# Kernel optimization log

Measured on AMD Instinct MI355X. Metric: run time of the kernel, lower is better.

The kernel has to match this reference:

```python
import jax, jax.numpy as jnp
import numpy as np

N_NODES = 50000
N_EDGES = 800000


def sage_conv(x, src, dst, Wl, b, Wr, n_nodes):
    # mean aggregation of source-node features into target nodes
    msg = x[src]                                            # [E, d]
    agg = jax.ops.segment_sum(msg, dst, num_segments=n_nodes)  # [N, d]
    cnt = jax.ops.segment_sum(jnp.ones((src.shape[0],), x.dtype), dst,
                              num_segments=n_nodes)         # [N]
    agg = agg / jnp.maximum(cnt, 1.0)[:, None]
    # out = lin_l(mean_aggr) + lin_r(x); bias only on lin_l (PyG default)
    return agg @ Wl.T + b + x @ Wr.T


def setup_inputs() -> dict:
    key = jax.random.key(0)
    ks = jax.random.split(key, 10)
    d_in, d_h, d_out = 128, 128, 64
    sc = lambda k, shp: jax.random.normal(k, shp, jnp.float32) * (1.0 / np.sqrt(shp[-1]))
    return {
        "x": jax.random.normal(ks[0], (N_NODES, d_in), jnp.float32),
        "edge_index": jax.random.randint(ks[1], (2, N_EDGES), 0, N_NODES, jnp.int64),
        "W1l": sc(ks[2], (d_h, d_in)), "b1": jnp.zeros((d_h,), jnp.float32),
        "W1r": sc(ks[3], (d_h, d_in)),
        "W2l": sc(ks[4], (d_h, d_h)), "b2": jnp.zeros((d_h,), jnp.float32),
        "W2r": sc(ks[5], (d_h, d_h)),
        "W3l": sc(ks[6], (d_out, d_h)), "b3": jnp.zeros((d_out,), jnp.float32),
        "W3r": sc(ks[7], (d_out, d_h)),
    }


def reference(x, edge_index, W1l, b1, W1r, W2l, b2, W2r, W3l, b3, W3r):
    src, dst = edge_index[0], edge_index[1]
    n = x.shape[0]
    # layer 1 + relu (dropout is identity in eval mode)
    h = jax.nn.relu(sage_conv(x, src, dst, W1l, b1, W1r, n))
    # layer 2 + relu
    h = jax.nn.relu(sage_conv(h, src, dst, W2l, b2, W2r, n))
    # final layer, no activation
    return sage_conv(h, src, dst, W3l, b3, W3r, n)
```

## Files before the change

### kernel.cpp

```cpp
#include <hip/hip_runtime.h>
#include <hip/hip_bf16.h>

#define DIN 128

typedef __attribute__((ext_vector_type(8))) short short8;
typedef __attribute__((ext_vector_type(4))) float f32x4;
typedef __attribute__((ext_vector_type(4))) unsigned short ushort4v;
typedef __attribute__((ext_vector_type(8))) unsigned short ushort8v;

__device__ __forceinline__ unsigned short f2bf(float f) {
    unsigned int u = __float_as_uint(f);
    u += 0x7FFFu + ((u >> 16) & 1u);
    return (unsigned short)(u >> 16);
}
__device__ __forceinline__ float bflo(unsigned int v) { return __uint_as_float(v << 16); }
__device__ __forceinline__ float bfhi(unsigned int v) { return __uint_as_float(v & 0xFFFF0000u); }

#define PAD 32
#define CHUNK 4096

__device__ __forceinline__ void pack_w_body(const float* __restrict__ Wl,
                                            const float* __restrict__ Wr,
                                            unsigned short* __restrict__ Wp, int NT, int idx) {
    if (idx >= NT * 8 * 64) return;
    int l = idx & 63;
    int ts = idx >> 6;
    int ks = ts & 7;
    int nt = ts >> 3;
    int row = nt * 16 + (l & 15);
    int k = ks * 32 + ((l >> 4) << 3);
    const float* s = (k < 128) ? (Wl + (size_t)row * 128 + k)
                               : (Wr + (size_t)row * 128 + (k - 128));
    float4 v0 = *reinterpret_cast<const float4*>(s);
    float4 v1 = *reinterpret_cast<const float4*>(s + 4);
    unsigned short* d = Wp + (size_t)idx * 8;
    ushort4v o0 = {f2bf(v0.x), f2bf(v0.y), f2bf(v0.z), f2bf(v0.w)};
    ushort4v o1 = {f2bf(v1.x), f2bf(v1.y), f2bf(v1.z), f2bf(v1.w)};
    *reinterpret_cast<ushort4v*>(d) = o0;
    *reinterpret_cast<ushort4v*>(d + 4) = o1;
}

__global__ __launch_bounds__(256) void prep_kernel(
    const float* __restrict__ x, unsigned short* __restrict__ xb,
    const float* __restrict__ W1l, const float* __restrict__ W1r, unsigned short* __restrict__ Wp1,
    const float* __restrict__ W2l, const float* __restrict__ W2r, unsigned short* __restrict__ Wp2,
    const float* __restrict__ W3l, const float* __restrict__ W3r, unsigned short* __restrict__ Wp3,
    const int* __restrict__ dst, int* __restrict__ bcnt, int E, int n, int CB) {
    __shared__ int h[256];
    int t = threadIdx.x;
    int b = blockIdx.x;
    if (b < CB) {
        int i = b * 256 + t;
        if (i < n * 16) {
            int node = i >> 4;
            int f0 = (i & 15) << 3;
            const float* s = x + (size_t)node * DIN + f0;
            float4 v0 = *reinterpret_cast<const float4*>(s);
            float4 v1 = *reinterpret_cast<const float4*>(s + 4);
            ushort8v o = {f2bf(v0.x), f2bf(v0.y), f2bf(v0.z), f2bf(v0.w),
                          f2bf(v1.x), f2bf(v1.y), f2bf(v1.z), f2bf(v1.w)};
            *reinterpret_cast<ushort8v*>(xb + (size_t)(f0 >> 5) * n * 32 +
                                         (size_t)node * 32 + (f0 & 31)) = o;
        }
        return;
    }
    b -= CB;
    if (b < 16) { pack_w_body(W1l, W1r, Wp1, 8, b * 256 + t); return; }
    b -= 16;
    if (b < 16) { pack_w_body(W2l, W2r, Wp2, 8, b * 256 + t); return; }
    b -= 16;
    if (b < 8) { pack_w_body(W3l, W3r, Wp3, 4, b * 256 + t); return; }
    b -= 8;
    h[t] = 0;
    __syncthreads();
    for (int i = b * 256 + t; i < E; i += 784 * 256)
        atomicAdd(&h[dst[i] >> 8], 1);
    __syncthreads();
    if (h[t] > 0) atomicAdd(&bcnt[t * PAD], h[t]);
}

__global__ __launch_bounds__(256) void bucket_scan_kernel(const int* __restrict__ bcnt,
                                                          int* __restrict__ bbase,
                                                          int* __restrict__ bcur,
                                                          int* __restrict__ row_ptr,
                                                          int nb, int n, int E) {
    __shared__ int s[256];
    int t = threadIdx.x;
    int v = (t < nb) ? bcnt[t * PAD] : 0;
    s[t] = v;
    __syncthreads();
    for (int off = 1; off < 256; off <<= 1) {
        int add = (t >= off) ? s[t - off] : 0;
        __syncthreads();
        s[t] += add;
        __syncthreads();
    }
    int excl = s[t] - v;
    bbase[t] = excl;
    bcur[t * PAD] = excl;
    if (t == 255) {
        bbase[256] = s[255];
        row_ptr[n] = E;
    }
}

__global__ __launch_bounds__(256) void chunk_scatter_kernel(const int* __restrict__ src,
                                                            const int* __restrict__ dst,
                                                            int* __restrict__ bcur,
                                                            unsigned int* __restrict__ tmp,
                                                            int E) {
    __shared__ int hist[256];
    __shared__ int base[256];
    int t = threadIdx.x;
    int e0 = blockIdx.x * CHUNK;
    int e1 = min(e0 + CHUNK, E);
    hist[t] = 0;
    __syncthreads();
    for (int e = e0 + t; e < e1; e += 256) {
        atomicAdd(&hist[dst[e] >> 8], 1);
    }
    __syncthreads();
    int hh = hist[t];
    if (hh > 0) base[t] = atomicAdd(&bcur[t * PAD], hh);
    __syncthreads();
    hist[t] = 0;
    __syncthreads();
    for (int e = e0 + t; e < e1; e += 256) {
        int d = dst[e];
        int bb = d >> 8;
        int p = base[bb] + atomicAdd(&hist[bb], 1);
        tmp[p] = (unsigned int)src[e] | ((unsigned int)(d & 255) << 16);
    }
}

__global__ __launch_bounds__(256) void bucket_fill_kernel(const unsigned int* __restrict__ tmp,
                                                          const int* __restrict__ bbase,
                                                          int* __restrict__ row_ptr,
                                                          unsigned short* __restrict__ col,
                                                          int n) {
    int b = blockIdx.x;
    int node0 = b << 8;
    int nn = min(256, n - node0);
    int begB = bbase[b], endB = bbase[b + 1];
    __shared__ int s[256];
    __shared__ int cur[256];
    int t = threadIdx.x;
    s[t] = 0;
    __syncthreads();
    for (int i = begB + t; i < endB; i += 256)
        atomicAdd(&s[(tmp[i] >> 16) & 255], 1);
    __syncthreads();
    int v = s[t];
    __syncthreads();
    for (int off = 1; off < 256; off <<= 1) {
        int add = (t >= off) ? s[t - off] : 0;
        __syncthreads();
        s[t] += add;
        __syncthreads();
    }
    int r = begB + s[t] - v;
    if (t < nn) row_ptr[node0 + t] = r;
    cur[t] = r;
    __syncthreads();
    for (int i = begB + t; i < endB; i += 256) {
        unsigned int e = tmp[i];
        int p = atomicAdd(&cur[(e >> 16) & 255], 1);
        col[p] = (unsigned short)(e & 0xFFFFu);
    }
}

__global__ __launch_bounds__(256) void aggregate_kernel(const unsigned short* __restrict__ feat,
                                                        const int* __restrict__ row_ptr,
                                                        const unsigned short* __restrict__ col,
                                                        unsigned short* __restrict__ agg,
                                                        int n, int nbn2) {
    int b = blockIdx.x;
    int chunk = (b >> 1) & 3;
    int nb = (b >> 3) * 2 + (b & 1);
    int lane = threadIdx.x & 63;
    int wave = threadIdx.x >> 6;
    int q = lane >> 4;
    int node = nb * 16 + wave * 4 + q;
    int slot = (lane >> 2) & 3;
    int fb = (lane & 3) << 3;
    size_t cs = (size_t)n * 32;
    const unsigned short* fc = feat + (size_t)chunk * cs;

    int beg = 0, end = 0;
    if (node < n) { beg = row_ptr[node]; end = row_ptr[node + 1]; }
    float a0 = 0.f, a1 = 0.f, a2 = 0.f, a3 = 0.f, a4 = 0.f, a5 = 0.f, a6 = 0.f, a7 = 0.f;
    int e = beg + slot;
    for (; e + 4 < end; e += 8) {
        int c0 = col[e];
        int c1 = col[e + 4];
        uint4 v0 = *reinterpret_cast<const uint4*>(fc + (size_t)c0 * 32 + fb);
        uint4 v1 = *reinterpret_cast<const uint4*>(fc + (size_t)c1 * 32 + fb);
        a0 += bflo(v0.x); a1 += bfhi(v0.x); a2 += bflo(v0.y); a3 += bfhi(v0.y);
        a4 += bflo(v0.z); a5 += bfhi(v0.z); a6 += bflo(v0.w); a7 += bfhi(v0.w);
        a0 += bflo(v1.x); a1 += bfhi(v1.x); a2 += bflo(v1.y); a3 += bfhi(v1.y);
        a4 += bflo(v1.z); a5 += bfhi(v1.z); a6 += bflo(v1.w); a7 += bfhi(v1.w);
    }
    if (e < end) {
        int c0 = col[e];
        uint4 v0 = *reinterpret_cast<const uint4*>(fc + (size_t)c0 * 32 + fb);
        a0 += bflo(v0.x); a1 += bfhi(v0.x); a2 += bflo(v0.y); a3 += bfhi(v0.y);
        a4 += bflo(v0.z); a5 += bfhi(v0.z); a6 += bflo(v0.w); a7 += bfhi(v0.w);
    }
    a0 += __shfl_xor(a0, 4); a1 += __shfl_xor(a1, 4); a2 += __shfl_xor(a2, 4);
    a3 += __shfl_xor(a3, 4); a4 += __shfl_xor(a4, 4); a5 += __shfl_xor(a5, 4);
    a6 += __shfl_xor(a6, 4); a7 += __shfl_xor(a7, 4);
    a0 += __shfl_xor(a0, 8); a1 += __shfl_xor(a1, 8); a2 += __shfl_xor(a2, 8);
    a3 += __shfl_xor(a3, 8); a4 += __shfl_xor(a4, 8); a5 += __shfl_xor(a5, 8);
    a6 += __shfl_xor(a6, 8); a7 += __shfl_xor(a7, 8);
    if (slot == 0 && node < n) {
        float sc = 1.0f / fmaxf((float)(end - beg), 1.0f);
        ushort8v o = {f2bf(a0 * sc), f2bf(a1 * sc), f2bf(a2 * sc), f2bf(a3 * sc),
                      f2bf(a4 * sc), f2bf(a5 * sc), f2bf(a6 * sc), f2bf(a7 * sc)};
        *reinterpret_cast<ushort8v*>(agg + (size_t)chunk * cs + (size_t)node * 32 + fb) = o;
    }
}

template <int DOUT, bool RELU, bool OUTBF>
__global__ __launch_bounds__(256, 4) void mfma_gemm_kernel(
    const unsigned short* __restrict__ aggb, const unsigned short* __restrict__ xb,
    const unsigned short* __restrict__ Wp, const float* __restrict__ bias,
    void* __restrict__ outv, int n) {
    constexpr int NT = DOUT / 16;
    const int lane = threadIdx.x & 63;
    const int wave = threadIdx.x >> 6;
    const int row0 = blockIdx.x * 64 + wave * 16;
    const int ar = row0 + (lane & 15);
    const int kg = (lane >> 4) << 3;
    const bool ok = ar < n;
    const size_t cs = (size_t)n * 32;

    const short8 z = {0, 0, 0, 0, 0, 0, 0, 0};
    short8 a[8];
    const unsigned short* arow = aggb + (size_t)ar * 32 + kg;
    const unsigned short* xrow = xb + (size_t)ar * 32 + kg;
#pragma unroll
    for (int ks = 0; ks < 4; ks++)
        a[ks] = ok ? *reinterpret_cast<const short8*>(arow + ks * cs) : z;
#pragma unroll
    for (int ks = 0; ks < 4; ks++)
        a[4 + ks] = ok ? *reinterpret_cast<const short8*>(xrow + ks * cs) : z;

    f32x4 acc[NT];
#pragma unroll
    for (int nt = 0; nt < NT; nt++) acc[nt] = {0.f, 0.f, 0.f, 0.f};

    const unsigned short* wp = Wp + ((size_t)lane << 3);
#pragma unroll
    for (int nt = 0; nt < NT; nt++) {
#pragma unroll
        for (int ks = 0; ks < 8; ks++) {
            short8 b = *reinterpret_cast<const short8*>(wp + ((size_t)(nt * 8 + ks) << 9));
            acc[nt] = __builtin_amdgcn_mfma_f32_16x16x32_bf16(a[ks], b, acc[nt], 0, 0, 0);
        }
    }

    const int orow0 = row0 + ((lane >> 4) << 2);
#pragma unroll
    for (int nt = 0; nt < NT; nt++) {
        int c = nt * 16 + (lane & 15);
        float bv = bias[c];
#pragma unroll
        for (int rg = 0; rg < 4; rg++) {
            int rr = orow0 + rg;
            if (rr < n) {
                float v = acc[nt][rg] + bv;
                if (RELU) v = fmaxf(v, 0.f);
                if (OUTBF) {
                    reinterpret_cast<unsigned short*>(outv)[(size_t)(nt >> 1) * cs +
                                                            (size_t)rr * 32 +
                                                            ((nt & 1) * 16 + (lane & 15))] =
                        f2bf(v);
                } else {
                    reinterpret_cast<float*>(outv)[(size_t)rr * DOUT + c] = v;
                }
            }
        }
    }
}

extern "C" void kernel_launch(void* const* d_in, const int* in_sizes, int n_in,
                              void* d_out, int out_size, void* d_ws, size_t ws_size,
                              hipStream_t stream) {
    const float* x = (const float*)d_in[0];
    const int* ei = (const int*)d_in[1];
    const float* W1l = (const float*)d_in[2];
    const float* b1 = (const float*)d_in[3];
    const float* W1r = (const float*)d_in[4];
    const float* W2l = (const float*)d_in[5];
    const float* b2 = (const float*)d_in[6];
    const float* W2r = (const float*)d_in[7];
    const float* W3l = (const float*)d_in[8];
    const float* b3 = (const float*)d_in[9];
    const float* W3r = (const float*)d_in[10];
    float* out = (float*)d_out;

    const int n = in_sizes[0] / DIN;
    const int E = in_sizes[1] / 2;
    const int* src = ei;
    const int* dst = ei + E;

    char* p = (char*)d_ws;
    auto take = [&](size_t bytes) {
        char* r = p;
        p += (bytes + 255) & ~(size_t)255;
        return r;
    };
    int* bcnt = (int*)take(256 * PAD * 4);
    int* bcur = (int*)take(256 * PAD * 4);
    int* bbase = (int*)take(257 * 4);
    int* row_ptr = (int*)take(((size_t)n + 1) * 4);
    unsigned int* tmp = (unsigned int*)take((size_t)E * 4);
    unsigned short* col = (unsigned short*)take((size_t)E * 2);
    unsigned short* xb = (unsigned short*)take((size_t)n * DIN * 2);
    unsigned short* aggb = (unsigned short*)take((size_t)n * DIN * 2);
    unsigned short* h1b = (unsigned short*)take((size_t)n * DIN * 2);
    unsigned short* h2b = (unsigned short*)take((size_t)n * DIN * 2);
    unsigned short* Wp1 = (unsigned short*)take(128 * 256 * 2);
    unsigned short* Wp2 = (unsigned short*)take(128 * 256 * 2);
    unsigned short* Wp3 = (unsigned short*)take(64 * 256 * 2);

    const int n_buckets = (n + 255) / 256;
    const int nbn = (n + 15) / 16;
    const int nbn2 = (nbn + 1) & ~1;
    const int nb_agg = 4 * nbn2;
    const int nb_gemm = (n + 63) / 64;
    const int nb_chunk = (E + CHUNK - 1) / CHUNK;
    const int CB = (n * 16 + 255) / 256;
    const int nb_prep = CB + 16 + 16 + 8 + 784;

    hipMemsetAsync(bcnt, 0, 256 * PAD * 4, stream);
    prep_kernel<<<nb_prep, 256, 0, stream>>>(x, xb, W1l, W1r, Wp1, W2l, W2r, Wp2,
                                             W3l, W3r, Wp3, dst, bcnt, E, n, CB);

    bucket_scan_kernel<<<1, 256, 0, stream>>>(bcnt, bbase, bcur, row_ptr, n_buckets, n, E);
    chunk_scatter_kernel<<<nb_chunk, 256, 0, stream>>>(src, dst, bcur, tmp, E);
    bucket_fill_kernel<<<n_buckets, 256, 0, stream>>>(tmp, bbase, row_ptr, col, n);

    aggregate_kernel<<<nb_agg, 256, 0, stream>>>(xb, row_ptr, col, aggb, n, nbn2);
    mfma_gemm_kernel<128, true, true><<<nb_gemm, 256, 0, stream>>>(aggb, xb, Wp1, b1, h1b, n);

    aggregate_kernel<<<nb_agg, 256, 0, stream>>>(h1b, row_ptr, col, aggb, n, nbn2);
    mfma_gemm_kernel<128, true, true><<<nb_gemm, 256, 0, stream>>>(aggb, h1b, Wp2, b2, h2b, n);

    aggregate_kernel<<<nb_agg, 256, 0, stream>>>(h2b, row_ptr, col, aggb, n, nbn2);
    mfma_gemm_kernel<64, false, false><<<nb_gemm, 256, 0, stream>>>(aggb, h2b, Wp3, b3, out, n);
}
```

Baseline: 187.4 us.

## Transform before aggregating in final layer and fold bucket scan into CSR kernels

The final SAGE layer now applies both weight matrices first: W3l·h goes to a 64-wide bf16 buffer and W3r·h + bias to a float buffer. A new agg_add kernel then mean-aggregates the 64-wide projected features and adds the residual, halving the width of the last gather. The separate single-block bucket scan kernel is removed; each scatter and fill block recomputes the small 256-entry prefix scan, and bcur becomes a zero-initialised relative offset. The aggregation loop is also unrolled to four gathers per iteration for more memory-level parallelism. In exchange the last layer rounds the projected messages to bf16 before averaging, and every block does redundant scan work.

```diff
diff --git a/kernel.cpp b/kernel.cpp
--- a/kernel.cpp
+++ b/kernel.cpp
@@ -79,39 +79,26 @@
     if (h[t] > 0) atomicAdd(&bcnt[t * PAD], h[t]);
 }
 
-__global__ __launch_bounds__(256) void bucket_scan_kernel(const int* __restrict__ bcnt,
-                                                          int* __restrict__ bbase,
-                                                          int* __restrict__ bcur,
-                                                          int* __restrict__ row_ptr,
-                                                          int nb, int n, int E) {
-    __shared__ int s[256];
-    int t = threadIdx.x;
-    int v = (t < nb) ? bcnt[t * PAD] : 0;
-    s[t] = v;
-    __syncthreads();
-    for (int off = 1; off < 256; off <<= 1) {
-        int add = (t >= off) ? s[t - off] : 0;
-        __syncthreads();
-        s[t] += add;
-        __syncthreads();
-    }
-    int excl = s[t] - v;
-    bbase[t] = excl;
-    bcur[t * PAD] = excl;
-    if (t == 255) {
-        bbase[256] = s[255];
-        row_ptr[n] = E;
-    }
-}
-
 __global__ __launch_bounds__(256) void chunk_scatter_kernel(const int* __restrict__ src,
                                                             const int* __restrict__ dst,
+                                                            const int* __restrict__ bcnt,
                                                             int* __restrict__ bcur,
                                                             unsigned int* __restrict__ tmp,
-                                                            int E) {
+                                                            int E, int nb_total) {
+    __shared__ int sc[256];
+    __shared__ int base[256];
     __shared__ int hist[256];
-    __shared__ int base[256];
     int t = threadIdx.x;
+    int v = (t < nb_total) ? bcnt[t * PAD] : 0;
+    sc[t] = v;
+    __syncthreads();
+    for (int off = 1; off < 256; off <<= 1) {
+        int add = (t >= off) ? sc[t - off] : 0;
+        __syncthreads();
+        sc[t] += add;
+        __syncthreads();
+    }
+    int excl = sc[t] - v;
     int e0 = blockIdx.x * CHUNK;
     int e1 = min(e0 + CHUNK, E);
     hist[t] = 0;
@@ -121,7 +108,7 @@
     }
     __syncthreads();
     int hh = hist[t];
-    if (hh > 0) base[t] = atomicAdd(&bcur[t * PAD], hh);
+    if (hh > 0) base[t] = excl + atomicAdd(&bcur[t * PAD], hh);
     __syncthreads();
     hist[t] = 0;
     __syncthreads();
@@ -134,31 +121,42 @@
 }
 
 __global__ __launch_bounds__(256) void bucket_fill_kernel(const unsigned int* __restrict__ tmp,
-                                                          const int* __restrict__ bbase,
+                                                          const int* __restrict__ bcnt,
                                                           int* __restrict__ row_ptr,
                                                           unsigned short* __restrict__ col,
-                                                          int n) {
+                                                          int n, int nb_total, int E) {
     int b = blockIdx.x;
     int node0 = b << 8;
     int nn = min(256, n - node0);
-    int begB = bbase[b], endB = bbase[b + 1];
-    __shared__ int s[256];
+    __shared__ int sc[256];
     __shared__ int cur[256];
     int t = threadIdx.x;
-    s[t] = 0;
+    int v = (t < nb_total) ? bcnt[t * PAD] : 0;
+    sc[t] = v;
+    __syncthreads();
+    for (int off = 1; off < 256; off <<= 1) {
+        int add = (t >= off) ? sc[t - off] : 0;
+        __syncthreads();
+        sc[t] += add;
+        __syncthreads();
+    }
+    int begB = (b == 0) ? 0 : sc[b - 1];
+    int endB = sc[b];
+    __syncthreads();
+    sc[t] = 0;
     __syncthreads();
     for (int i = begB + t; i < endB; i += 256)
-        atomicAdd(&s[(tmp[i] >> 16) & 255], 1);
-    __syncthreads();
-    int v = s[t];
+        atomicAdd(&sc[(tmp[i] >> 16) & 255], 1);
+    __syncthreads();
+    int dv = sc[t];
     __syncthreads();
     for (int off = 1; off < 256; off <<= 1) {
-        int add = (t >= off) ? s[t - off] : 0;
-        __syncthreads();
-        s[t] += add;
-        __syncthreads();
-    }
-    int r = begB + s[t] - v;
+        int add = (t >= off) ? sc[t - off] : 0;
+        __syncthreads();
+        sc[t] += add;
+        __syncthreads();
+    }
+    int r = begB + sc[t] - dv;
     if (t < nn) row_ptr[node0 + t] = r;
     cur[t] = r;
     __syncthreads();
@@ -167,13 +165,14 @@
         int p = atomicAdd(&cur[(e >> 16) & 255], 1);
         col[p] = (unsigned short)(e & 0xFFFFu);
     }
+    if (b == 0 && t == 0) row_ptr[n] = E;
 }
 
 __global__ __launch_bounds__(256) void aggregate_kernel(const unsigned short* __restrict__ feat,
                                                         const int* __restrict__ row_ptr,
                                                         const unsigned short* __restrict__ col,
                                                         unsigned short* __restrict__ agg,
-                                                        int n, int nbn2) {
+                                                        int n) {
     int b = blockIdx.x;
     int chunk = (b >> 1) & 3;
     int nb = (b >> 3) * 2 + (b & 1);
@@ -190,17 +189,25 @@
     if (node < n) { beg = row_ptr[node]; end = row_ptr[node + 1]; }
     float a0 = 0.f, a1 = 0.f, a2 = 0.f, a3 = 0.f, a4 = 0.f, a5 = 0.f, a6 = 0.f, a7 = 0.f;
     int e = beg + slot;
-    for (; e + 4 < end; e += 8) {
+    for (; e + 12 < end; e += 16) {
         int c0 = col[e];
         int c1 = col[e + 4];
+        int c2 = col[e + 8];
+        int c3 = col[e + 12];
         uint4 v0 = *reinterpret_cast<const uint4*>(fc + (size_t)c0 * 32 + fb);
         uint4 v1 = *reinterpret_cast<const uint4*>(fc + (size_t)c1 * 32 + fb);
+        uint4 v2 = *reinterpret_cast<const uint4*>(fc + (size_t)c2 * 32 + fb);
+        uint4 v3 = *reinterpret_cast<const uint4*>(fc + (size_t)c3 * 32 + fb);
         a0 += bflo(v0.x); a1 += bfhi(v0.x); a2 += bflo(v0.y); a3 += bfhi(v0.y);
         a4 += bflo(v0.z); a5 += bfhi(v0.z); a6 += bflo(v0.w); a7 += bfhi(v0.w);
         a0 += bflo(v1.x); a1 += bfhi(v1.x); a2 += bflo(v1.y); a3 += bfhi(v1.y);
         a4 += bflo(v1.z); a5 += bfhi(v1.z); a6 += bflo(v1.w); a7 += bfhi(v1.w);
-    }
-    if (e < end) {
+        a0 += bflo(v2.x); a1 += bfhi(v2.x); a2 += bflo(v2.y); a3 += bfhi(v2.y);
+        a4 += bflo(v2.z); a5 += bfhi(v2.z); a6 += bflo(v2.w); a7 += bfhi(v2.w);
+        a0 += bflo(v3.x); a1 += bfhi(v3.x); a2 += bflo(v3.y); a3 += bfhi(v3.y);
+        a4 += bflo(v3.z); a5 += bfhi(v3.z); a6 += bflo(v3.w); a7 += bfhi(v3.w);
+    }
+    for (; e < end; e += 4) {
         int c0 = col[e];
         uint4 v0 = *reinterpret_cast<const uint4*>(fc + (size_t)c0 * 32 + fb);
         a0 += bflo(v0.x); a1 += bfhi(v0.x); a2 += bflo(v0.y); a3 += bfhi(v0.y);
@@ -220,12 +227,11 @@
     }
 }
 
-template <int DOUT, bool RELU, bool OUTBF>
 __global__ __launch_bounds__(256, 4) void mfma_gemm_kernel(
     const unsigned short* __restrict__ aggb, const unsigned short* __restrict__ xb,
     const unsigned short* __restrict__ Wp, const float* __restrict__ bias,
-    void* __restrict__ outv, int n) {
-    constexpr int NT = DOUT / 16;
+    unsigned short* __restrict__ outv, int n) {
+    constexpr int NT = 8;
     const int lane = threadIdx.x & 63;
     const int wave = threadIdx.x >> 6;
     const int row0 = blockIdx.x * 64 + wave * 16;
@@ -268,18 +274,126 @@
         for (int rg = 0; rg < 4; rg++) {
             int rr = orow0 + rg;
             if (rr < n) {
-                float v = acc[nt][rg] + bv;
-                if (RELU) v = fmaxf(v, 0.f);
-                if (OUTBF) {
-                    reinterpret_cast<unsigned short*>(outv)[(size_t)(nt >> 1) * cs +
-                                                            (size_t)rr * 32 +
-                                                            ((nt & 1) * 16 + (lane & 15))] =
-                        f2bf(v);
-                } else {
-                    reinterpret_cast<float*>(outv)[(size_t)rr * DOUT + c] = v;
-                }
+                float v = fmaxf(acc[nt][rg] + bv, 0.f);
+                outv[(size_t)(nt >> 1) * cs + (size_t)rr * 32 + ((nt & 1) * 16 + (lane & 15))] =
+                    f2bf(v);
             }
         }
+    }
+}
+
+__global__ __launch_bounds__(256, 4) void gemm3_kernel(
+    const unsigned short* __restrict__ h2, const unsigned short* __restrict__ Wp3,
+    const float* __restrict__ bias, unsigned short* __restrict__ y3l,
+    float* __restrict__ y3r, int n) {
+    const int lane = threadIdx.x & 63;
+    const int wave = threadIdx.x >> 6;
+    const int row0 = blockIdx.x * 64 + wave * 16;
+    const int ar = row0 + (lane & 15);
+    const int kg = (lane >> 4) << 3;
+    const bool ok = ar < n;
+    const size_t cs = (size_t)n * 32;
+    const size_t cs2 = (size_t)n * 32;
+
+    const short8 z = {0, 0, 0, 0, 0, 0, 0, 0};
+    short8 a[4];
+    const unsigned short* xrow = h2 + (size_t)ar * 32 + kg;
+#pragma unroll
+    for (int ks = 0; ks < 4; ks++)
+        a[ks] = ok ? *reinterpret_cast<const short8*>(xrow + ks * cs) : z;
+
+    f32x4 accL[4], accR[4];
+#pragma unroll
+    for (int nt = 0; nt < 4; nt++) { accL[nt] = {0.f, 0.f, 0.f, 0.f}; accR[nt] = {0.f, 0.f, 0.f, 0.f}; }
+
+    const unsigned short* wp = Wp3 + ((size_t)lane << 3);
+#pragma unroll
+    for (int nt = 0; nt < 4; nt++) {
+#pragma unroll
+        for (int ks = 0; ks < 4; ks++) {
+            short8 bl = *reinterpret_cast<const short8*>(wp + ((size_t)(nt * 8 + ks) << 9));
+            accL[nt] = __builtin_amdgcn_mfma_f32_16x16x32_bf16(a[ks], bl, accL[nt], 0, 0, 0);
+            short8 br = *reinterpret_cast<const short8*>(wp + ((size_t)(nt * 8 + 4 + ks) << 9));
+            accR[nt] = __builtin_amdgcn_mfma_f32_16x16x32_bf16(a[ks], br, accR[nt], 0, 0, 0);
+        }
+    }
+
+    const int orow0 = row0 + ((lane >> 4) << 2);
+#pragma unroll
+    for (int nt = 0; nt < 4; nt++) {
+        int c = nt * 16 + (lane & 15);
+        float bv = bias[c];
+#pragma unroll
+        for (int rg = 0; rg < 4; rg++) {
+            int rr = orow0 + rg;
+            if (rr < n) {
+                y3l[(size_t)(nt >> 1) * cs2 + (size_t)rr * 32 + ((nt & 1) * 16 + (lane & 15))] =
+                    f2bf(accL[nt][rg]);
+                y3r[(size_t)rr * 64 + c] = accR[nt][rg] + bv;
+            }
+        }
+    }
+}
+
+__global__ __launch_bounds__(256) void agg_add_kernel(const unsigned short* __restrict__ y3l,
+                                                      const float* __restrict__ y3r,
+                                                      const int* __restrict__ row_ptr,
+                                                      const unsigned short* __restrict__ col,
+                                                      float* __restrict__ out, int n) {
+    int b = blockIdx.x;
+    int chunk = (b >> 2) & 1;
+    int nb = (b >> 3) * 4 + (b & 3);
+    int lane = threadIdx.x & 63;
+    int wave = threadIdx.x >> 6;
+    int q = lane >> 4;
+    int node = nb * 16 + wave * 4 + q;
+    int slot = (lane >> 2) & 3;
+    int fb = (lane & 3) << 3;
+    size_t cs = (size_t)n * 32;
+    const unsigned short* fc = y3l + (size_t)chunk * cs;
+
+    int beg = 0, end = 0;
+    if (node < n) { beg = row_ptr[node]; end = row_ptr[node + 1]; }
+    float a0 = 0.f, a1 = 0.f, a2 = 0.f, a3 = 0.f, a4 = 0.f, a5 = 0.f, a6 = 0.f, a7 = 0.f;
+    int e = beg + slot;
+    for (; e + 12 < end; e += 16) {
+        int c0 = col[e];
+        int c1 = col[e + 4];
+        int c2 = col[e + 8];
+        int c3 = col[e + 12];
+        uint4 v0 = *reinterpret_cast<const uint4*>(fc + (size_t)c0 * 32 + fb);
+        uint4 v1 = *reinterpret_cast<const uint4*>(fc + (size_t)c1 * 32 + fb);
+        uint4 v2 = *reinterpret_cast<const uint4*>(fc + (size_t)c2 * 32 + fb);
+        uint4 v3 = *reinterpret_cast<const uint4*>(fc + (size_t)c3 * 32 + fb);
+        a0 += bflo(v0.x); a1 += bfhi(v0.x); a2 += bflo(v0.y); a3 += bfhi(v0.y);
+        a4 += bflo(v0.z); a5 += bfhi(v0.z); a6 += bflo(v0.w); a7 += bfhi(v0.w);
+        a0 += bflo(v1.x); a1 += bfhi(v1.x); a2 += bflo(v1.y); a3 += bfhi(v1.y);
+        a4 += bflo(v1.z); a5 += bfhi(v1.z); a6 += bflo(v1.w); a7 += bfhi(v1.w);
+        a0 += bflo(v2.x); a1 += bfhi(v2.x); a2 += bflo(v2.y); a3 += bfhi(v2.y);
+        a4 += bflo(v2.z); a5 += bfhi(v2.z); a6 += bflo(v2.w); a7 += bfhi(v2.w);
+        a0 += bflo(v3.x); a1 += bfhi(v3.x); a2 += bflo(v3.y); a3 += bfhi(v3.y);
+        a4 += bflo(v3.z); a5 += bfhi(v3.z); a6 += bflo(v3.w); a7 += bfhi(v3.w);
+    }
+    for (; e < end; e += 4) {
+        int c0 = col[e];
+        uint4 v0 = *reinterpret_cast<const uint4*>(fc + (size_t)c0 * 32 + fb);
+        a0 += bflo(v0.x); a1 += bfhi(v0.x); a2 += bflo(v0.y); a3 += bfhi(v0.y);
+        a4 += bflo(v0.z); a5 += bfhi(v0.z); a6 += bflo(v0.w); a7 += bfhi(v0.w);
+    }
+    a0 += __shfl_xor(a0, 4); a1 += __shfl_xor(a1, 4); a2 += __shfl_xor(a2, 4);
+    a3 += __shfl_xor(a3, 4); a4 += __shfl_xor(a4, 4); a5 += __shfl_xor(a5, 4);
+    a6 += __shfl_xor(a6, 4); a7 += __shfl_xor(a7, 4);
+    a0 += __shfl_xor(a0, 8); a1 += __shfl_xor(a1, 8); a2 += __shfl_xor(a2, 8);
+    a3 += __shfl_xor(a3, 8); a4 += __shfl_xor(a4, 8); a5 += __shfl_xor(a5, 8);
+    a6 += __shfl_xor(a6, 8); a7 += __shfl_xor(a7, 8);
+    if (slot == 0 && node < n) {
+        float sc = 1.0f / fmaxf((float)(end - beg), 1.0f);
+        const float* yr = y3r + (size_t)node * 64 + chunk * 32 + fb;
+        float* o = out + (size_t)node * 64 + chunk * 32 + fb;
+        float4 r0 = make_float4(a0 * sc + yr[0], a1 * sc + yr[1], a2 * sc + yr[2], a3 * sc + yr[3]);
+        float4 r1 = make_float4(a4 * sc + yr[4], a5 * sc + yr[5], a6 * sc + yr[6], a7 * sc + yr[7]);
+        *reinterpret_cast<float4*>(o) = r0;
+        *reinterpret_cast<float4*>(o + 4) = r1;
     }
 }
 
@@ -312,7 +426,6 @@
     };
     int* bcnt = (int*)take(256 * PAD * 4);
     int* bcur = (int*)take(256 * PAD * 4);
-    int* bbase = (int*)take(257 * 4);
     int* row_ptr = (int*)take(((size_t)n + 1) * 4);
     unsigned int* tmp = (unsigned int*)take((size_t)E * 4);
     unsigned short* col = (unsigned short*)take((size_t)E * 2);
@@ -320,6 +433,8 @@
     unsigned short* aggb = (unsigned short*)take((size_t)n * DIN * 2);
     unsigned short* h1b = (unsigned short*)take((size_t)n * DIN * 2);
     unsigned short* h2b = (unsigned short*)take((size_t)n * DIN * 2);
+    unsigned short* y3l = (unsigned short*)take((size_t)n * 64 * 2);
+    float* y3r = (float*)take((size_t)n * 64 * 4);
     unsigned short* Wp1 = (unsigned short*)take(128 * 256 * 2);
     unsigned short* Wp2 = (unsigned short*)take(128 * 256 * 2);
     unsigned short* Wp3 = (unsigned short*)take(64 * 256 * 2);
@@ -328,25 +443,26 @@
     const int nbn = (n + 15) / 16;
     const int nbn2 = (nbn + 1) & ~1;
     const int nb_agg = 4 * nbn2;
+    const int nbn4 = (nbn + 3) & ~3;
+    const int nb_agg3 = 2 * nbn4;
     const int nb_gemm = (n + 63) / 64;
     const int nb_chunk = (E + CHUNK - 1) / CHUNK;
     const int CB = (n * 16 + 255) / 256;
     const int nb_prep = CB + 16 + 16 + 8 + 784;
 
-    hipMemsetAsync(bcnt, 0, 256 * PAD * 4, stream);
+    hipMemsetAsync(bcnt, 0, 2 * 256 * PAD * 4, stream);
     prep_kernel<<<nb_prep, 256, 0, stream>>>(x, xb, W1l, W1r, Wp1, W2l, W2r, Wp2,
                                              W3l, W3r, Wp3, dst, bcnt, E, n, CB);
 
-    bucket_scan_kernel<<<1, 256, 0, stream>>>(bcnt, bbase, bcur, row_ptr, n_buckets, n, E);
-    chunk_scatter_kernel<<<nb_chunk, 256, 0, stream>>>(src, dst, bcur, tmp, E);
-    bucket_fill_kernel<<<n_buckets, 256, 0, stream>>>(tmp, bbase, row_ptr, col, n);
-
-    aggregate_kernel<<<nb_agg, 256, 0, stream>>>(xb, row_ptr, col, aggb, n, nbn2);
-    mfma_gemm_kernel<128, true, true><<<nb_gemm, 256, 0, stream>>>(aggb, xb, Wp1, b1, h1b, n);
-
-    aggregate_kernel<<<nb_agg, 256, 0, stream>>>(h1b, row_ptr, col, aggb, n, nbn2);
-    mfma_gemm_kernel<128, true, true><<<nb_gemm, 256, 0, stream>>>(aggb, h1b, Wp2, b2, h2b, n);
-
-    aggregate_kernel<<<nb_agg, 256, 0, stream>>>(h2b, row_ptr, col, aggb, n, nbn2);
-    mfma_gemm_kernel<64, false, false><<<nb_gemm, 256, 0, stream>>>(aggb, h2b, Wp3, b3, out, n);
-}
+    chunk_scatter_kernel<<<nb_chunk, 256, 0, stream>>>(src, dst, bcnt, bcur, tmp, E, n_buckets);
+    bucket_fill_kernel<<<n_buckets, 256, 0, stream>>>(tmp, bcnt, row_ptr, col, n, n_buckets, E);
+
+    aggregate_kernel<<<nb_agg, 256, 0, stream>>>(xb, row_ptr, col, aggb, n);
+    mfma_gemm_kernel<<<nb_gemm, 256, 0, stream>>>(aggb, xb, Wp1, b1, h1b, n);
+
+    aggregate_kernel<<<nb_agg, 256, 0, stream>>>(h1b, row_ptr, col, aggb, n);
+    mfma_gemm_kernel<<<nb_gemm, 256, 0, stream>>>(aggb, h1b, Wp2, b2, h2b, n);
+
+    gemm3_kernel<<<nb_gemm, 256, 0, stream>>>(h2b, Wp3, b3, y3l, y3r, n);
+    agg_add_kernel<<<nb_agg3, 256, 0, stream>>>(y3l, y3r, row_ptr, col, out, n);
+}
```

New measurement: 179.4 us. 4.3% less time.
